# Kernel tuning notes

Hardware: AMD Instinct MI355X
Metric: run time of the kernel (lower is better)

Reference implementation:

```python
import jax, jax.numpy as jnp
import numpy as np

B, S, H, F, E, TOP_K = 8, 1024, 1024, 3584, 8, 2


def setup_inputs() -> dict:
    key = jax.random.key(0)
    ks = jax.random.split(key, 10)
    hidden_states = jax.random.normal(ks[0], (B, S, H), jnp.float32)
    gate_w = jax.random.normal(ks[1], (E, H), jnp.float32) * 0.02
    # int8 weights stored as int-valued fp32 (symmetric quantized), per-output-channel scales
    w1_q = jnp.round(jnp.clip(jax.random.normal(ks[2], (E, F, H)) * 40.0, -127.0, 127.0))
    w1_s = jax.random.uniform(ks[3], (E, F), minval=1e-4, maxval=1e-3)
    w3_q = jnp.round(jnp.clip(jax.random.normal(ks[4], (E, F, H)) * 40.0, -127.0, 127.0))
    w3_s = jax.random.uniform(ks[5], (E, F), minval=1e-4, maxval=1e-3)
    w2_q = jnp.round(jnp.clip(jax.random.normal(ks[6], (E, H, F)) * 40.0, -127.0, 127.0))
    w2_s = jax.random.uniform(ks[7], (E, H), minval=1e-4, maxval=1e-3)
    # static per-expert input scale for the down projection (W8A8...WithQuantScale)
    down_scale = jax.random.uniform(ks[8], (E,), minval=0.01, maxval=0.05)
    return {"hidden_states": hidden_states, "gate_w": gate_w,
            "w1_q": w1_q, "w1_s": w1_s, "w3_q": w3_q, "w3_s": w3_s,
            "w2_q": w2_q, "w2_s": w2_s, "down_scale": down_scale}


def _quant_per_token(x):
    # symmetric per-token dynamic int8 quantization (act_quant='per-token')
    s = jnp.maximum(jnp.max(jnp.abs(x), axis=-1, keepdims=True), 1e-8) / 127.0
    q = jnp.clip(jnp.round(x / s), -127.0, 127.0)
    return q, s


def reference(hidden_states, gate_w, w1_q, w1_s, w3_q, w3_s, w2_q, w2_s, down_scale):
    b, s, h = hidden_states.shape
    x = hidden_states.reshape(b * s, h)              # [T, H]
    # --- router: softmax over experts, top-2, renormalize ---
    router_logits = x @ gate_w.T                     # [T, E]
    probs = jax.nn.softmax(router_logits.astype(jnp.float32), axis=-1)
    top_w, top_idx = jax.lax.top_k(probs, TOP_K)     # [T, 2]
    top_w = top_w / jnp.sum(top_w, axis=-1, keepdims=True)
    T = x.shape[0]
    # dense [T, E] routing weights (zero for unselected experts)
    w_dense = jnp.zeros((T, E), probs.dtype).at[jnp.arange(T)[:, None], top_idx].add(top_w)
    # --- quantize activations once (expert-independent per-token quant) ---
    x_q, x_s = _quant_per_token(x)
    out = jnp.zeros((T, h), jnp.float32)
    for e in range(E):  # fixed small expert count
        h1 = (x_q @ w1_q[e].T) * x_s * w1_s[e]       # [T, F] dequantized gate proj
        h3 = (x_q @ w3_q[e].T) * x_s * w3_s[e]       # [T, F] dequantized up proj
        g = jax.nn.silu(h1) * h3                     # SwiGLU
        g_q = jnp.clip(jnp.round(g / down_scale[e]), -127.0, 127.0)  # static-scale quant
        y = (g_q @ w2_q[e].T) * (down_scale[e] * w2_s[e])            # [T, H]
        out = out + w_dense[:, e:e + 1] * y
    return out.reshape(b, s, h), router_logits
```

## Files before the change

### kernel.cpp

```cpp
#include <hip/hip_runtime.h>
#include <stdint.h>

typedef int v4i  __attribute__((ext_vector_type(4)));
typedef int v16i __attribute__((ext_vector_type(16)));

#define T_TOK 8192
#define H_DIM 1024
#define F_DIM 3584
#define N_EXP 8

#define W13T_OFF  0u
#define XQ_OFF    58720256u
#define W2T_OFF   67108864u
#define GBT_OFF   96501760u
#define XS_OFF    158892032u
#define LIST_OFF  158924800u
#define TW_OFF    159186944u
#define TSLOT_OFF 159449088u
#define CNT_OFF   159514624u
#define OFFS_OFF  159514656u
#define NT_OFF    159514688u
#define WLIST_OFF 159514752u
#define XG_OFF    67108864u
#define XSG_OFF   84934656u
#define YBUF_OFF  0u

__device__ __forceinline__ void async16(const void* g, void* l) {
    __builtin_amdgcn_global_load_lds(
        (const __attribute__((address_space(1))) unsigned int*)g,
        (__attribute__((address_space(3))) unsigned int*)l, 16, 0, 0);
}

__device__ __forceinline__ int pack4(float a, float b, float c, float d) {
    int ia = (int)(signed char)(int)a, ib = (int)(signed char)(int)b;
    int ic = (int)(signed char)(int)c, id = (int)(signed char)(int)d;
    return (ia & 0xff) | ((ib & 0xff) << 8) | ((ic & 0xff) << 16) | (id << 24);
}

__global__ __launch_bounds__(256) void convert13_kernel(
    const float* __restrict__ w1, const float* __restrict__ w3,
    v4i* __restrict__ w13t)
{
    int d = blockIdx.x * 256 + threadIdx.x;
    int wi = d & 511;
    int rg = wi >> 7, c16 = (wi >> 5) & 3, r = wi & 31;
    int si = d >> 9;
    int mat = si & 1, kt = (si >> 1) & 15, rest = si >> 5;
    int e = rest / 28, ft = rest - e * 28;
    const float* s = (mat ? w3 : w1)
      + ((size_t)(e * F_DIM + ft * 128 + rg * 32 + r)) * H_DIM
      + kt * 64 + c16 * 16;
    const float4* sv = (const float4*)s;
    float4 f0 = sv[0], f1 = sv[1], f2 = sv[2], f3 = sv[3];
    v4i o;
    o.x = pack4(f0.x, f0.y, f0.z, f0.w);
    o.y = pack4(f1.x, f1.y, f1.z, f1.w);
    o.z = pack4(f2.x, f2.y, f2.z, f2.w);
    o.w = pack4(f3.x, f3.y, f3.z, f3.w);
    w13t[d] = o;
}

__global__ __launch_bounds__(256) void convert2_kernel(
    const float* __restrict__ w2, v4i* __restrict__ w2t)
{
    int d = blockIdx.x * 256 + threadIdx.x;
    int wi = d & 511;
    int rg = wi >> 7, c16 = (wi >> 5) & 3, r = wi & 31;
    int si = d >> 9;
    int kt = si % 56, q = si / 56;
    int ht = q & 7, e = q >> 3;
    const float* s = w2 + ((size_t)(e * H_DIM + ht * 128 + rg * 32 + r)) * F_DIM
          + kt * 64 + c16 * 16;
    const float4* sv = (const float4*)s;
    float4 f0 = sv[0], f1 = sv[1], f2 = sv[2], f3 = sv[3];
    v4i o;
    o.x = pack4(f0.x, f0.y, f0.z, f0.w);
    o.y = pack4(f1.x, f1.y, f1.z, f1.w);
    o.z = pack4(f2.x, f2.y, f2.z, f2.w);
    o.w = pack4(f3.x, f3.y, f3.z, f3.w);
    w2t[d] = o;
}

__global__ __launch_bounds__(256) void router_kernel(
    const float* __restrict__ x, const float* __restrict__ gw,
    int8_t* __restrict__ xq, float* __restrict__ xs,
    int* __restrict__ cnt, int* __restrict__ list, float* __restrict__ tw,
    int* __restrict__ tslot, float* __restrict__ logits_out)
{
    const int token = blockIdx.x;
    const int t = threadIdx.x;
    __shared__ float red[256 * 8];
    __shared__ float ram[256];
    __shared__ float s_scale;

    const float4 xv = ((const float4*)(x + (size_t)token * H_DIM))[t];
    float am = fmaxf(fmaxf(fabsf(xv.x), fabsf(xv.y)), fmaxf(fabsf(xv.z), fabsf(xv.w)));
    float part[8];
#pragma unroll
    for (int e = 0; e < 8; e++) {
        const float4 g = ((const float4*)(gw + e * H_DIM))[t];
        part[e] = xv.x * g.x + xv.y * g.y + xv.z * g.z + xv.w * g.w;
    }
#pragma unroll
    for (int e = 0; e < 8; e++) red[t * 8 + e] = part[e];
    ram[t] = am;
    __syncthreads();
    for (int s = 128; s > 0; s >>= 1) {
        if (t < s) {
#pragma unroll
            for (int e = 0; e < 8; e++) red[t * 8 + e] += red[(t + s) * 8 + e];
            ram[t] = fmaxf(ram[t], ram[t + s]);
        }
        __syncthreads();
    }
    if (t == 0) {
        float l[8];
#pragma unroll
        for (int e = 0; e < 8; e++) l[e] = red[e];
        float m = l[0];
#pragma unroll
        for (int e = 1; e < 8; e++) m = fmaxf(m, l[e]);
        float p[8], sum = 0.0f;
#pragma unroll
        for (int e = 0; e < 8; e++) { p[e] = expf(l[e] - m); sum += p[e]; }
#pragma unroll
        for (int e = 0; e < 8; e++) p[e] = p[e] / sum;
        int i0 = 0;
#pragma unroll
        for (int e = 1; e < 8; e++) if (p[e] > p[i0]) i0 = e;
        int i1 = (i0 == 0) ? 1 : 0;
#pragma unroll
        for (int e = 0; e < 8; e++) if (e != i0 && p[e] > p[i1]) i1 = e;
        float tsum = p[i0] + p[i1];
        float w0 = p[i0] / tsum;
        float w1 = p[i1] / tsum;
#pragma unroll
        for (int e = 0; e < 8; e++) logits_out[(size_t)token * 8 + e] = l[e];
        int pos0 = atomicAdd(&cnt[i0], 1);
        list[i0 * T_TOK + pos0] = token;  tw[i0 * T_TOK + pos0] = w0;
        int pos1 = atomicAdd(&cnt[i1], 1);
        list[i1 * T_TOK + pos1] = token;  tw[i1 * T_TOK + pos1] = w1;
        tslot[token * 2 + 0] = (i0 << 16) | pos0;
        tslot[token * 2 + 1] = (i1 << 16) | pos1;
        s_scale = fmaxf(ram[0], 1e-8f) / 127.0f;
        xs[token] = s_scale;
    }
    __syncthreads();
    const float s = s_scale;
    char4 c;
    c.x = (signed char)fminf(fmaxf(rintf(xv.x / s), -127.0f), 127.0f);
    c.y = (signed char)fminf(fmaxf(rintf(xv.y / s), -127.0f), 127.0f);
    c.z = (signed char)fminf(fmaxf(rintf(xv.z / s), -127.0f), 127.0f);
    c.w = (signed char)fminf(fmaxf(rintf(xv.w / s), -127.0f), 127.0f);
    ((char4*)xq)[(size_t)token * (H_DIM / 4) + t] = c;
}

__global__ void planner_kernel(const int* __restrict__ cnt, int* __restrict__ offs,
                               int* __restrict__ ntile, int* __restrict__ wlist)
{
    if (threadIdx.x == 0) {
        int s = 0, nt = 0;
        for (int e = 0; e < N_EXP; e++) {
            offs[e] = s;
            int c = cnt[e];
            s += c;
            int tc = (c + 127) >> 7;
            for (int m = 0; m < tc; m++) wlist[nt++] = (e << 8) | m;
        }
        *ntile = nt;
    }
}

__global__ __launch_bounds__(256) void gather_kernel(
    const int8_t* __restrict__ xq, const float* __restrict__ xs,
    const int* __restrict__ cnt, const int* __restrict__ ntile_p,
    const int* __restrict__ wlist, const int* __restrict__ list,
    v4i* __restrict__ xg, float* __restrict__ xsg)
{
    const int bx = blockIdx.x;
    if (bx >= *ntile_p) return;
    const int wl = wlist[bx];
    const int e = wl >> 8, mt = wl & 255;
    const int count = cnt[e];
    const int cm1 = count - 1;
    const int t = threadIdx.x;
    const int* liste = list + e * T_TOK;
    __shared__ int stok[128];
    if (t < 128) {
        int p = mt * 128 + t;
        int tok = liste[p < count ? p : cm1];
        stok[t] = tok;
        xsg[bx * 128 + t] = xs[tok];
    }
    __syncthreads();
    v4i* dslab = xg + (size_t)bx * 8192;
#pragma unroll
    for (int i = 0; i < 32; i++) {
        int flat = i * 256 + t;
        int row = flat >> 6, c = flat & 63;
        v4i v = ((const v4i*)(xq + (size_t)stok[row] * H_DIM))[c];
        int kt = c >> 2, c16 = c & 3, rg = row >> 5, r = row & 31;
        dslab[kt * 512 + rg * 128 + c16 * 32 + r] = v;
    }
}

__global__ __launch_bounds__(256, 2) void gemm1_kernel(
    const v4i* __restrict__ xg, const float* __restrict__ xsg,
    const v4i* __restrict__ w13t,
    const float* __restrict__ w1s, const float* __restrict__ w3s,
    const float* __restrict__ dscale,
    const int* __restrict__ cnt, const int* __restrict__ ntile_p,
    const int* __restrict__ wlist,
    int8_t* __restrict__ gbt)
{
    const int bx = blockIdx.x;
    if (bx >= *ntile_p) return;
    const int wl = wlist[bx];
    const int e = wl >> 8, mt = wl & 255;
    const int ft = blockIdx.y;
    const int count = cnt[e];
    const int t = threadIdx.x, lane = t & 63, w = t >> 6;
    const int wm = w >> 1, wn = w & 1;

    __shared__ v4i sm[3072];
    char* smb = (char*)sm;

    const char* gA = (const char*)(xg + (size_t)bx * 8192) + w * 2048 + lane * 16;
    const char* gB = (const char*)(w13t + (size_t)(e * 28 + ft) * 16384) + lane * 16;
    const int wq = w * 2048;

    v16i acc1[2][2], acc3[2][2];
#pragma unroll
    for (int i = 0; i < 2; i++)
#pragma unroll
        for (int j = 0; j < 2; j++)
#pragma unroll
            for (int r = 0; r < 16; r++) { acc1[i][j][r] = 0; acc3[i][j][r] = 0; }

    auto stage = [&](int kt, int buf) {
        char* base = smb + buf * 24576;
        const char* sa = gA + kt * 8192;
        async16(sa,        base + wq);
        async16(sa + 1024, base + wq + 1024);
        const char* s1 = gB + (size_t)kt * 16384;
        async16(s1 + wq,               base + 8192 + wq);
        async16(s1 + wq + 1024,        base + 8192 + wq + 1024);
        async16(s1 + 8192 + wq,        base + 16384 + wq);
        async16(s1 + 8192 + wq + 1024, base + 16384 + wq + 1024);
    };
    auto compute = [&](int buf) {
        const v4i* S = sm + buf * 1536;
#pragma unroll
        for (int ks = 0; ks < 2; ks++) {
            const int base = (2 * ks + (lane >> 5)) * 32 + (lane & 31);
            v4i a0  = S[base + (wm * 2 + 0) * 128];
            v4i a1  = S[base + (wm * 2 + 1) * 128];
            v4i b1a = S[512 + base + (wn * 2 + 0) * 128];
            v4i b1b = S[512 + base + (wn * 2 + 1) * 128];
            v4i b3a = S[1024 + base + (wn * 2 + 0) * 128];
            v4i b3b = S[1024 + base + (wn * 2 + 1) * 128];
            acc1[0][0] = __builtin_amdgcn_mfma_i32_32x32x32_i8(a0, b1a, acc1[0][0], 0, 0, 0);
            acc1[0][1] = __builtin_amdgcn_mfma_i32_32x32x32_i8(a0, b1b, acc1[0][1], 0, 0, 0);
            acc1[1][0] = __builtin_amdgcn_mfma_i32_32x32x32_i8(a1, b1a, acc1[1][0], 0, 0, 0);
            acc1[1][1] = __builtin_amdgcn_mfma_i32_32x32x32_i8(a1, b1b, acc1[1][1], 0, 0, 0);
            acc3[0][0] = __builtin_amdgcn_mfma_i32_32x32x32_i8(a0, b3a, acc3[0][0], 0, 0, 0);
            acc3[0][1] = __builtin_amdgcn_mfma_i32_32x32x32_i8(a0, b3b, acc3[0][1], 0, 0, 0);
            acc3[1][0] = __builtin_amdgcn_mfma_i32_32x32x32_i8(a1, b3a, acc3[1][0], 0, 0, 0);
            acc3[1][1] = __builtin_amdgcn_mfma_i32_32x32x32_i8(a1, b3b, acc3[1][1], 0, 0, 0);
        }
    };

    stage(0, 0);
    for (int kt = 0; kt < 16; kt++) {
        __syncthreads();
        if (kt + 1 < 16) stage(kt + 1, (kt + 1) & 1);
        compute(kt & 1);
    }

    const float ds = dscale[e];
    const float rds = 1.0f / ds;
    int8_t* gout = gbt + (size_t)bx * 458752 + (size_t)(ft * 2 + wn) * 8192;
#pragma unroll
    for (int im = 0; im < 2; im++) {
#pragma unroll
        for (int in = 0; in < 2; in++) {
            const int fco = in * 32 + (lane & 31);
            const int fcol = ft * 128 + wn * 64 + fco;
            const float s1 = w1s[e * F_DIM + fcol];
            const float s3 = w3s[e * F_DIM + fcol];
            const int coff = ((in * 2 + ((lane & 31) >> 4)) * 32) * 16 + (lane & 15);
#pragma unroll
            for (int r = 0; r < 16; r++) {
                int row = wm * 64 + im * 32 + (r & 3) + 8 * (r >> 2) + 4 * (lane >> 5);
                int p = mt * 128 + row;
                if (p < count) {
                    float sx = xsg[bx * 128 + row];
                    float h1 = (float)acc1[im][in][r] * sx * s1;
                    float h3 = (float)acc3[im][in][r] * sx * s3;
                    float g = h1 * __builtin_amdgcn_rcpf(1.0f + __expf(-h1)) * h3;
                    float qv = fminf(fmaxf(rintf(g * rds), -127.0f), 127.0f);
                    gout[(size_t)((wm * 2 + im) * 128 + (row & 31)) * 16 + coff] = (int8_t)qv;
                }
            }
        }
    }
}

__global__ __launch_bounds__(256, 3) void gemm2_kernel(
    const int8_t* __restrict__ gbt, const v4i* __restrict__ w2t,
    const float* __restrict__ w2s, const float* __restrict__ dscale,
    const int* __restrict__ cnt, const int* __restrict__ offs,
    const int* __restrict__ ntile_p, const int* __restrict__ wlist,
    const float* __restrict__ tw, float* __restrict__ ybuf)
{
    const int bx = blockIdx.x;
    if (bx >= *ntile_p) return;
    const int wl = wlist[bx];
    const int e = wl >> 8, mt = wl & 255;
    const int ht = blockIdx.y;
    const int count = cnt[e];
    const int t = threadIdx.x, lane = t & 63, w = t >> 6;
    const int wm = w >> 1, wn = w & 1;

    __shared__ v4i sm[2048];
    char* smb = (char*)sm;

    const char* gA = (const char*)gbt + (size_t)bx * 458752 + w * 2048 + lane * 16;
    const char* gB = (const char*)(w2t + (size_t)(e * 8 + ht) * 28672) + w * 2048 + lane * 16;

    v16i acc[2][2];
#pragma unroll
    for (int i = 0; i < 2; i++)
#pragma unroll
        for (int j = 0; j < 2; j++)
#pragma unroll
            for (int r = 0; r < 16; r++) acc[i][j][r] = 0;

    auto stage = [&](int kt, int buf) {
        char* base = smb + buf * 16384;
        const size_t ko = (size_t)kt * 8192;
        async16(gA + ko,        base + w * 2048);
        async16(gA + ko + 1024, base + w * 2048 + 1024);
        async16(gB + ko,        base + 8192 + w * 2048);
        async16(gB + ko + 1024, base + 8192 + w * 2048 + 1024);
    };
    auto compute = [&](int buf) {
        const v4i* S = sm + buf * 1024;
#pragma unroll
        for (int ks = 0; ks < 2; ks++) {
            const int base = (2 * ks + (lane >> 5)) * 32 + (lane & 31);
            v4i a0 = S[base + (wm * 2 + 0) * 128];
            v4i a1 = S[base + (wm * 2 + 1) * 128];
            v4i b0 = S[512 + base + (wn * 2 + 0) * 128];
            v4i b1 = S[512 + base + (wn * 2 + 1) * 128];
            acc[0][0] = __builtin_amdgcn_mfma_i32_32x32x32_i8(a0, b0, acc[0][0], 0, 0, 0);
            acc[0][1] = __builtin_amdgcn_mfma_i32_32x32x32_i8(a0, b1, acc[0][1], 0, 0, 0);
            acc[1][0] = __builtin_amdgcn_mfma_i32_32x32x32_i8(a1, b0, acc[1][0], 0, 0, 0);
            acc[1][1] = __builtin_amdgcn_mfma_i32_32x32x32_i8(a1, b1, acc[1][1], 0, 0, 0);
        }
    };

    stage(0, 0);
    for (int kt = 0; kt < 56; kt++) {
        __syncthreads();
        if (kt + 1 < 56) stage(kt + 1, (kt + 1) & 1);
        compute(kt & 1);
    }

    const float ds = dscale[e];
    const int rowbase = offs[e] + mt * 128;
#pragma unroll
    for (int im = 0; im < 2; im++) {
#pragma unroll
        for (int in = 0; in < 2; in++) {
            const int h = ht * 128 + wn * 64 + in * 32 + (lane & 31);
            const float sc = ds * w2s[e * H_DIM + h];
#pragma unroll
            for (int r = 0; r < 16; r++) {
                int row = wm * 64 + im * 32 + (r & 3) + 8 * (r >> 2) + 4 * (lane >> 5);
                int p = mt * 128 + row;
                if (p < count) {
                    float rw = tw[e * T_TOK + p];
                    ybuf[(size_t)(rowbase + row) * H_DIM + h] = (float)acc[im][in][r] * sc * rw;
                }
            }
        }
    }
}

__global__ __launch_bounds__(256) void combine_kernel(
    const float* __restrict__ ybuf, const int* __restrict__ offs,
    const int* __restrict__ tslot, float* __restrict__ out)
{
    const int token = blockIdx.x;
    const int i = threadIdx.x;
    const int s0 = tslot[token * 2 + 0];
    const int s1 = tslot[token * 2 + 1];
    const int slot0 = offs[s0 >> 16] + (s0 & 0xffff);
    const int slot1 = offs[s1 >> 16] + (s1 & 0xffff);
    float4 a = ((const float4*)(ybuf + (size_t)slot0 * H_DIM))[i];
    float4 b = ((const float4*)(ybuf + (size_t)slot1 * H_DIM))[i];
    float4 o;
    o.x = a.x + b.x; o.y = a.y + b.y; o.z = a.z + b.z; o.w = a.w + b.w;
    ((float4*)(out + (size_t)token * H_DIM))[i] = o;
}

extern "C" void kernel_launch(void* const* d_in, const int* in_sizes, int n_in,
                              void* d_out, int out_size, void* d_ws, size_t ws_size,
                              hipStream_t stream)
{
    const float* x    = (const float*)d_in[0];
    const float* gw   = (const float*)d_in[1];
    const float* w1   = (const float*)d_in[2];
    const float* w1s  = (const float*)d_in[3];
    const float* w3   = (const float*)d_in[4];
    const float* w3s  = (const float*)d_in[5];
    const float* w2   = (const float*)d_in[6];
    const float* w2s  = (const float*)d_in[7];
    const float* dsc  = (const float*)d_in[8];

    float* out = (float*)d_out;
    float* logits_out = out + (size_t)T_TOK * H_DIM;

    char* ws = (char*)d_ws;
    v4i*    w13t = (v4i*)   (ws + W13T_OFF);
    int8_t* xq   = (int8_t*)(ws + XQ_OFF);
    v4i*    w2t  = (v4i*)   (ws + W2T_OFF);
    int8_t* gbt  = (int8_t*)(ws + GBT_OFF);
    float*  xs   = (float*) (ws + XS_OFF);
    int*    list = (int*)   (ws + LIST_OFF);
    float*  tws  = (float*) (ws + TW_OFF);
    int*    tslot= (int*)   (ws + TSLOT_OFF);
    int*    cnt  = (int*)   (ws + CNT_OFF);
    int*    offs = (int*)   (ws + OFFS_OFF);
    int*    ntile= (int*)   (ws + NT_OFF);
    int*    wlist= (int*)   (ws + WLIST_OFF);
    v4i*    xg   = (v4i*)   (ws + XG_OFF);
    float*  xsg  = (float*) (ws + XSG_OFF);
    float*  ybuf = (float*) (ws + YBUF_OFF);

    hipMemsetAsync(cnt, 0, N_EXP * sizeof(int), stream);

    convert13_kernel<<<14336, 256, 0, stream>>>(w1, w3, w13t);
    router_kernel<<<T_TOK, 256, 0, stream>>>(x, gw, xq, xs, cnt, list, tws, tslot, logits_out);
    planner_kernel<<<1, 64, 0, stream>>>(cnt, offs, ntile, wlist);
    gather_kernel<<<136, 256, 0, stream>>>(xq, xs, cnt, ntile, wlist, list, xg, xsg);
    gemm1_kernel<<<dim3(136, 28), 256, 0, stream>>>(
        xg, xsg, w13t, w1s, w3s, dsc, cnt, ntile, wlist, gbt);
    convert2_kernel<<<7168, 256, 0, stream>>>(w2, w2t);
    gemm2_kernel<<<dim3(136, 8), 256, 0, stream>>>(
        gbt, w2t, w2s, dsc, cnt, offs, ntile, wlist, tws, ybuf);
    combine_kernel<<<T_TOK, 256, 0, stream>>>(ybuf, offs, tslot, out);
}
```

Before: 870.5 us.

## Replace global atomic routing with per-block histograms, prefix scan, and scatter pass

The router now processes one token per wavefront using shuffle reductions instead of a shared-memory tree, and computes top-2 weights directly from logits. Global atomicAdd on expert counters is replaced by per-block local histograms, followed by a single-block prefix-scan planner and a separate scatter kernel that writes the expert lists deterministically. This removes global atomic contention and the 8192-block launch, and drops the memset. The cost is two extra small kernel launches and some additional workspace traffic.

```diff
diff --git a/kernel.cpp b/kernel.cpp
--- a/kernel.cpp
+++ b/kernel.cpp
@@ -21,6 +21,9 @@
 #define OFFS_OFF  159514656u
 #define NT_OFF    159514688u
 #define WLIST_OFF 159514752u
+#define RINFO_OFF 96501760u
+#define WP_OFF    96534528u
+#define BHIST_OFF 96600064u
 #define XG_OFF    67108864u
 #define XSG_OFF   84934656u
 #define YBUF_OFF  0u
@@ -81,94 +84,149 @@
     w2t[d] = o;
 }
 
-__global__ __launch_bounds__(256) void router_kernel(
+__global__ __launch_bounds__(256, 4) void router_kernel(
     const float* __restrict__ x, const float* __restrict__ gw,
     int8_t* __restrict__ xq, float* __restrict__ xs,
-    int* __restrict__ cnt, int* __restrict__ list, float* __restrict__ tw,
-    int* __restrict__ tslot, float* __restrict__ logits_out)
-{
-    const int token = blockIdx.x;
+    int* __restrict__ bhist, int* __restrict__ rinfo, float2* __restrict__ wp,
+    float* __restrict__ logits_out)
+{
+    const int t = threadIdx.x, lane = t & 63, wv = t >> 6;
+    __shared__ int lhist[8];
+    if (t < 8) lhist[t] = 0;
+    __syncthreads();
+    const float4* gw4 = (const float4*)gw;
+#pragma unroll 1
+    for (int i = 0; i < 2; i++) {
+        const int token = blockIdx.x * 8 + wv * 2 + i;
+        const float4* xrow = (const float4*)(x + (size_t)token * H_DIM);
+        float4 xv[4];
+#pragma unroll
+        for (int j = 0; j < 4; j++) xv[j] = xrow[j * 64 + lane];
+        float am = 0.0f;
+#pragma unroll
+        for (int j = 0; j < 4; j++)
+            am = fmaxf(am, fmaxf(fmaxf(fabsf(xv[j].x), fabsf(xv[j].y)),
+                                 fmaxf(fabsf(xv[j].z), fabsf(xv[j].w))));
+        float l[8];
+#pragma unroll
+        for (int e = 0; e < 8; e++) {
+            float d = 0.0f;
+#pragma unroll
+            for (int j = 0; j < 4; j++) {
+                float4 g = gw4[e * 256 + j * 64 + lane];
+                d += xv[j].x * g.x + xv[j].y * g.y + xv[j].z * g.z + xv[j].w * g.w;
+            }
+            l[e] = d;
+        }
+#pragma unroll
+        for (int m = 1; m < 64; m <<= 1) {
+#pragma unroll
+            for (int e = 0; e < 8; e++) l[e] += __shfl_xor(l[e], m, 64);
+            am = fmaxf(am, __shfl_xor(am, m, 64));
+        }
+        float v0 = l[0]; int i0 = 0;
+#pragma unroll
+        for (int e = 1; e < 8; e++) if (l[e] > v0) { v0 = l[e]; i0 = e; }
+        float v1 = -3.4e38f; int i1 = 0;
+#pragma unroll
+        for (int e = 0; e < 8; e++) if (e != i0 && l[e] > v1) { v1 = l[e]; i1 = e; }
+        const float tt = __expf(v1 - v0);
+        const float w0 = 1.0f / (1.0f + tt);
+        const float w1 = tt * w0;
+        const float s = fmaxf(am, 1e-8f) / 127.0f;
+        const float rs = 1.0f / s;
+        int8_t* xqr = xq + (size_t)token * H_DIM;
+#pragma unroll
+        for (int j = 0; j < 4; j++) {
+            char4 c;
+            c.x = (signed char)fminf(fmaxf(rintf(xv[j].x * rs), -127.0f), 127.0f);
+            c.y = (signed char)fminf(fmaxf(rintf(xv[j].y * rs), -127.0f), 127.0f);
+            c.z = (signed char)fminf(fmaxf(rintf(xv[j].z * rs), -127.0f), 127.0f);
+            c.w = (signed char)fminf(fmaxf(rintf(xv[j].w * rs), -127.0f), 127.0f);
+            ((char4*)xqr)[j * 64 + lane] = c;
+        }
+        if (lane == 0) {
+            xs[token] = s;
+#pragma unroll
+            for (int e = 0; e < 8; e++) logits_out[(size_t)token * 8 + e] = l[e];
+            int r0 = atomicAdd(&lhist[i0], 1);
+            int r1 = atomicAdd(&lhist[i1], 1);
+            rinfo[token] = i0 | (i1 << 3) | (r0 << 6) | (r1 << 10);
+            wp[token] = make_float2(w0, w1);
+        }
+    }
+    __syncthreads();
+    if (t < 8) bhist[blockIdx.x * 8 + t] = lhist[t];
+}
+
+__global__ __launch_bounds__(256) void planner_kernel(
+    int* __restrict__ bhist, int* __restrict__ cnt, int* __restrict__ offs,
+    int* __restrict__ ntile, int* __restrict__ wlist)
+{
+    __shared__ int sm[8 * 1060];
+    __shared__ int tot[8];
     const int t = threadIdx.x;
-    __shared__ float red[256 * 8];
-    __shared__ float ram[256];
-    __shared__ float s_scale;
-
-    const float4 xv = ((const float4*)(x + (size_t)token * H_DIM))[t];
-    float am = fmaxf(fmaxf(fabsf(xv.x), fabsf(xv.y)), fmaxf(fabsf(xv.z), fabsf(xv.w)));
-    float part[8];
-#pragma unroll
-    for (int e = 0; e < 8; e++) {
-        const float4 g = ((const float4*)(gw + e * H_DIM))[t];
-        part[e] = xv.x * g.x + xv.y * g.y + xv.z * g.z + xv.w * g.w;
-    }
-#pragma unroll
-    for (int e = 0; e < 8; e++) red[t * 8 + e] = part[e];
-    ram[t] = am;
+#pragma unroll
+    for (int k = 0; k < 32; k++) {
+        int idx = k * 256 + t;
+        int v = bhist[idx];
+        int e = idx & 7, b = idx >> 3;
+        sm[e * 1060 + b + (b >> 5)] = v;
+    }
     __syncthreads();
-    for (int s = 128; s > 0; s >>= 1) {
-        if (t < s) {
-#pragma unroll
-            for (int e = 0; e < 8; e++) red[t * 8 + e] += red[(t + s) * 8 + e];
-            ram[t] = fmaxf(ram[t], ram[t + s]);
-        }
-        __syncthreads();
-    }
+    const int e = t >> 5, sub = t & 31;
+    int* seg = sm + e * 1060 + sub * 33;
+    int run = 0;
+#pragma unroll
+    for (int i = 0; i < 32; i++) { int v = seg[i]; seg[i] = run; run += v; }
+    int inc = run;
+#pragma unroll
+    for (int d = 1; d < 32; d <<= 1) {
+        int u = __shfl_up(inc, d, 32);
+        if (sub >= d) inc += u;
+    }
+    const int segbase = inc - run;
+    if (sub == 31) tot[e] = inc;
+#pragma unroll
+    for (int i = 0; i < 32; i++) seg[i] += segbase;
+    __syncthreads();
     if (t == 0) {
-        float l[8];
-#pragma unroll
-        for (int e = 0; e < 8; e++) l[e] = red[e];
-        float m = l[0];
-#pragma unroll
-        for (int e = 1; e < 8; e++) m = fmaxf(m, l[e]);
-        float p[8], sum = 0.0f;
-#pragma unroll
-        for (int e = 0; e < 8; e++) { p[e] = expf(l[e] - m); sum += p[e]; }
-#pragma unroll
-        for (int e = 0; e < 8; e++) p[e] = p[e] / sum;
-        int i0 = 0;
-#pragma unroll
-        for (int e = 1; e < 8; e++) if (p[e] > p[i0]) i0 = e;
-        int i1 = (i0 == 0) ? 1 : 0;
-#pragma unroll
-        for (int e = 0; e < 8; e++) if (e != i0 && p[e] > p[i1]) i1 = e;
-        float tsum = p[i0] + p[i1];
-        float w0 = p[i0] / tsum;
-        float w1 = p[i1] / tsum;
-#pragma unroll
-        for (int e = 0; e < 8; e++) logits_out[(size_t)token * 8 + e] = l[e];
-        int pos0 = atomicAdd(&cnt[i0], 1);
-        list[i0 * T_TOK + pos0] = token;  tw[i0 * T_TOK + pos0] = w0;
-        int pos1 = atomicAdd(&cnt[i1], 1);
-        list[i1 * T_TOK + pos1] = token;  tw[i1 * T_TOK + pos1] = w1;
-        tslot[token * 2 + 0] = (i0 << 16) | pos0;
-        tslot[token * 2 + 1] = (i1 << 16) | pos1;
-        s_scale = fmaxf(ram[0], 1e-8f) / 127.0f;
-        xs[token] = s_scale;
-    }
-    __syncthreads();
-    const float s = s_scale;
-    char4 c;
-    c.x = (signed char)fminf(fmaxf(rintf(xv.x / s), -127.0f), 127.0f);
-    c.y = (signed char)fminf(fmaxf(rintf(xv.y / s), -127.0f), 127.0f);
-    c.z = (signed char)fminf(fmaxf(rintf(xv.z / s), -127.0f), 127.0f);
-    c.w = (signed char)fminf(fmaxf(rintf(xv.w / s), -127.0f), 127.0f);
-    ((char4*)xq)[(size_t)token * (H_DIM / 4) + t] = c;
-}
-
-__global__ void planner_kernel(const int* __restrict__ cnt, int* __restrict__ offs,
-                               int* __restrict__ ntile, int* __restrict__ wlist)
-{
-    if (threadIdx.x == 0) {
         int s = 0, nt = 0;
-        for (int e = 0; e < N_EXP; e++) {
-            offs[e] = s;
-            int c = cnt[e];
+        for (int ee = 0; ee < 8; ee++) {
+            offs[ee] = s;
+            int c = tot[ee];
+            cnt[ee] = c;
             s += c;
             int tc = (c + 127) >> 7;
-            for (int m = 0; m < tc; m++) wlist[nt++] = (e << 8) | m;
+            for (int m = 0; m < tc; m++) wlist[nt++] = (ee << 8) | m;
         }
         *ntile = nt;
     }
+#pragma unroll
+    for (int k = 0; k < 32; k++) {
+        int idx = k * 256 + t;
+        int ee = idx & 7, b = idx >> 3;
+        bhist[idx] = sm[ee * 1060 + b + (b >> 5)];
+    }
+}
+
+__global__ __launch_bounds__(256) void scatter_kernel(
+    const int* __restrict__ bhist, const int* __restrict__ rinfo,
+    const float2* __restrict__ wp, int* __restrict__ list,
+    float* __restrict__ tw, int* __restrict__ tslot)
+{
+    const int token = blockIdx.x * 256 + threadIdx.x;
+    const int ri = rinfo[token];
+    const float2 wpr = wp[token];
+    const int b = token >> 3;
+    const int e0 = ri & 7, e1 = (ri >> 3) & 7;
+    const int r0 = (ri >> 6) & 15, r1 = (ri >> 10) & 15;
+    const int p0 = bhist[b * 8 + e0] + r0;
+    const int p1 = bhist[b * 8 + e1] + r1;
+    list[e0 * T_TOK + p0] = token;  tw[e0 * T_TOK + p0] = wpr.x;
+    list[e1 * T_TOK + p1] = token;  tw[e1 * T_TOK + p1] = wpr.y;
+    tslot[token * 2 + 0] = (e0 << 16) | p0;
+    tslot[token * 2 + 1] = (e1 << 16) | p1;
 }
 
 __global__ __launch_bounds__(256) void gather_kernel(
@@ -435,15 +493,17 @@
     int*    offs = (int*)   (ws + OFFS_OFF);
     int*    ntile= (int*)   (ws + NT_OFF);
     int*    wlist= (int*)   (ws + WLIST_OFF);
+    int*    rinfo= (int*)   (ws + RINFO_OFF);
+    float2* wp   = (float2*)(ws + WP_OFF);
+    int*    bhist= (int*)   (ws + BHIST_OFF);
     v4i*    xg   = (v4i*)   (ws + XG_OFF);
     float*  xsg  = (float*) (ws + XSG_OFF);
     float*  ybuf = (float*) (ws + YBUF_OFF);
 
-    hipMemsetAsync(cnt, 0, N_EXP * sizeof(int), stream);
-
     convert13_kernel<<<14336, 256, 0, stream>>>(w1, w3, w13t);
-    router_kernel<<<T_TOK, 256, 0, stream>>>(x, gw, xq, xs, cnt, list, tws, tslot, logits_out);
-    planner_kernel<<<1, 64, 0, stream>>>(cnt, offs, ntile, wlist);
+    router_kernel<<<1024, 256, 0, stream>>>(x, gw, xq, xs, bhist, rinfo, wp, logits_out);
+    planner_kernel<<<1, 256, 0, stream>>>(bhist, cnt, offs, ntile, wlist);
+    scatter_kernel<<<32, 256, 0, stream>>>(bhist, rinfo, wp, list, tws, tslot);
     gather_kernel<<<136, 256, 0, stream>>>(xq, xs, cnt, ntile, wlist, list, xg, xsg);
     gemm1_kernel<<<dim3(136, 28), 256, 0, stream>>>(
         xg, xsg, w13t, w1s, w3s, dsc, cnt, ntile, wlist, gbt);
```

New measurement: 749.2 us. -13.9%, faster.
